# Kernel tuning notes

Measured on AMD Instinct MI355X. Metric: run time of the kernel, lower is better.

Reference implementation:

```python
import jax, jax.numpy as jnp
import numpy as np

J = 15       # joints
D = 128      # per-joint feature dim
ANG = 3      # per-joint angle dim
EPS = 1e-12  # F.normalize eps
TEMP = 200.0
SCALE = 16.0


def setup_inputs() -> dict:
    key = jax.random.key(0)
    k1, k2 = jax.random.split(key)
    B, N, E = 16384, 68, J * D + J * ANG  # E = 1965
    emb = jax.random.normal(k1, (B, E), dtype=jnp.float32)
    W = jax.random.normal(k2, (N, E), dtype=jnp.float32)
    return {"emb": emb, "W": W}


def reference(emb, W):
    B = emb.shape[0]
    N = W.shape[0]
    # split feature / angle blocks
    x_feat = emb[:, : J * D].reshape(B, J, D)        # (B, 15, 128)
    x_ang = emb[:, J * D :].reshape(B, 1, J, ANG)    # (B, 1, 15, 3)
    p_feat = W[:, : J * D].reshape(N, J, D)          # (N, 15, 128)
    p_ang = W[:, J * D :].reshape(1, N, J, ANG)      # (1, N, 15, 3)

    # per-joint angle distance and (detached in torch) softmax weighting
    ang_w = jnp.linalg.norm(x_ang - p_ang, axis=-1)            # (B, N, 15)
    w2 = jax.nn.softmax(ang_w / TEMP, axis=-1) * J             # (B, N, 15)

    # NOTE: the torch code computes argsort(ang_w) but immediately overwrites the
    # index with an identity permutation (ind = [0..14]), so the gather is a no-op.
    # Hence normalization is over the flat 15*128 block per batch / per class.
    xn = x_feat / jnp.maximum(
        jnp.linalg.norm(x_feat.reshape(B, -1), axis=-1), EPS
    )[:, None, None]
    pn = p_feat / jnp.maximum(
        jnp.linalg.norm(p_feat.reshape(N, -1), axis=-1), EPS
    )[:, None, None]

    # per-joint cosine contributions, weighted and summed
    s = jnp.einsum("bjd,njd->bnj", xn, pn)                     # (B, N, 15)
    logit = (s * w2).sum(-1) * SCALE                           # (B, N)
    return logit
```

## Files before the change

### kernel.cpp

```cpp
#include <hip/hip_runtime.h>
#include <hip/hip_bf16.h>

typedef __bf16 bf16x8 __attribute__((ext_vector_type(8)));
typedef float  f32x4  __attribute__((ext_vector_type(4)));

static constexpr int E    = 1965;
static constexpr int KF   = 1920;
static constexpr int NJ   = 15;
static constexpr int NCLS = 68;
static constexpr int NPAD = 80;
static constexpr int NT   = 5;
static constexpr int NS   = 60;
static constexpr int CH   = 12;

static constexpr size_t PNF_BYTES = (size_t)NT * NS * 64 * 8 * 2;

__global__ __launch_bounds__(256) void prep_kernel(const float* __restrict__ W,
                                                   __bf16* __restrict__ pnf,
                                                   float* __restrict__ pa) {
    const int n = blockIdx.x;
    const int t = threadIdx.x;
    float v[8];
    float ss = 0.f;
    if (n < NCLS && t < 240) {
        const float* src = W + (size_t)n * E + 8 * t;
        #pragma unroll
        for (int i = 0; i < 8; ++i) { v[i] = src[i]; ss += v[i] * v[i]; }
    } else {
        #pragma unroll
        for (int i = 0; i < 8; ++i) v[i] = 0.f;
    }
    #pragma unroll
    for (int off = 32; off >= 1; off >>= 1) ss += __shfl_xor(ss, off);
    __shared__ float rbuf[4];
    if ((t & 63) == 0) rbuf[t >> 6] = ss;
    __syncthreads();
    const float total = rbuf[0] + rbuf[1] + rbuf[2] + rbuf[3];
    const float rnorm = 1.f / fmaxf(sqrtf(total), 1e-12f);

    if (t < 240) {
        bf16x8 o;
        #pragma unroll
        for (int i = 0; i < 8; ++i) o[i] = (__bf16)(v[i] * rnorm);
        const int s = t >> 2, g = t & 3;
        const int lane = (n & 15) + 16 * g;
        const size_t off = (((size_t)(n >> 4) * NS + s) * 64 + lane) * 8;
        *(bf16x8*)(pnf + off) = o;
    }
    if (t < 45) {
        pa[n * 45 + t] = (n < NCLS) ? W[(size_t)n * E + KF + t] : 0.f;
    }
}

__global__ __launch_bounds__(320) void cos_kernel(const float* __restrict__ emb,
                                                  const __bf16* __restrict__ pnf,
                                                  const float* __restrict__ pa,
                                                  float* __restrict__ out) {
    __shared__ float  Abuf[2][2560];
    __shared__ __bf16 Bbuf[2][25][512];
    __shared__ float  xa[16][48];

    const int tid = threadIdx.x;
    const int m0  = blockIdx.x * 16;
    const int w   = tid >> 6;
    const int l   = tid & 63;
    const int lr  = l & 15;
    const int lg  = l >> 4;

    for (int idx = tid; idx < 16 * 45; idx += 320) {
        const int r = idx / 45, c = idx - r * 45;
        xa[r][c] = emb[(size_t)(m0 + r) * E + KF + c];
    }

    const int gA   = l ^ ((l >> 3) & 7);
    const int arow = (gA >> 1) & 15;
    const float* srcA = emb + (size_t)(m0 + arow) * E + 8 * (gA >> 5) + 4 * (gA & 1)
                        + 32 * w;
    const __bf16* srcB = pnf + ((size_t)w * NS * 64 + l) * 8;

    #define ISSUE(c, buf)                                                               \
        {                                                                               \
            _Pragma("unroll")                                                           \
            for (int b_ = 0; b_ < 2; ++b_)                                              \
                __builtin_amdgcn_global_load_lds(                                       \
                    (const __attribute__((address_space(1))) void*)(srcA + 160 * (c) + 16 * b_), \
                    (__attribute__((address_space(3))) void*)&Abuf[buf][(2 * w + b_) * 256],     \
                    16, 0, 0);                                                          \
            _Pragma("unroll")                                                           \
            for (int s_ = 0; s_ < 5; ++s_)                                              \
                __builtin_amdgcn_global_load_lds(                                       \
                    (const __attribute__((address_space(1))) void*)(srcB + (5 * (c) + s_) * 512),\
                    (__attribute__((address_space(3))) void*)&Bbuf[buf][w * 5 + s_][0],          \
                    16, 0, 0);                                                          \
        }

    const int g0    = 32 * (lg & 1) + 2 * lr;
    const int p_lo  = g0 ^ ((g0 >> 3) & 7);
    const int p_hi  = p_lo ^ 1;
    const int aoff_lo = (lg >> 1) * 256 + 4 * p_lo;
    const int aoff_hi = (lg >> 1) * 256 + 4 * p_hi;

    f32x4 acc[NJ];
    #pragma unroll
    for (int j = 0; j < NJ; ++j) acc[j] = f32x4{0.f, 0.f, 0.f, 0.f};
    float ssq = 0.f;

    ISSUE(0, 0);

    #pragma unroll
    for (int c = 0; c < CH; ++c) {
        __syncthreads();
        if (c + 1 < CH) ISSUE(c + 1, (c + 1) & 1);

        #pragma unroll
        for (int s = 0; s < 5; ++s) {
            const f32x4 alo = *(const f32x4*)&Abuf[c & 1][s * 512 + aoff_lo];
            const f32x4 ahi = *(const f32x4*)&Abuf[c & 1][s * 512 + aoff_hi];
            const bf16x8 b  = *(const bf16x8*)&Bbuf[c & 1][w * 5 + s][l * 8];
            bf16x8 af;
            #pragma unroll
            for (int q = 0; q < 4; ++q) {
                ssq += alo[q] * alo[q] + ahi[q] * ahi[q];
                af[q]     = (__bf16)alo[q];
                af[4 + q] = (__bf16)ahi[q];
            }
            const int gk = 5 * c + s;
            acc[gk >> 2] = __builtin_amdgcn_mfma_f32_16x16x32_bf16(af, b, acc[gk >> 2], 0, 0, 0);
        }
    }
    #undef ISSUE

    ssq += __shfl_xor(ssq, 16);
    ssq += __shfl_xor(ssq, 32);

    const int r0  = lg * 4;
    const int col = w * 16 + lr;

    float rn[4];
    #pragma unroll
    for (int r = 0; r < 4; ++r)
        rn[r] = 240.f / fmaxf(sqrtf(__shfl(ssq, r0 + r)), 1e-12f);

    const float* pav = pa + col * 45;
    float num[4] = {0.f, 0.f, 0.f, 0.f};
    float den[4] = {0.f, 0.f, 0.f, 0.f};
    #pragma unroll
    for (int j = 0; j < NJ; ++j) {
        const float p0a = pav[3 * j + 0];
        const float p1a = pav[3 * j + 1];
        const float p2a = pav[3 * j + 2];
        #pragma unroll
        for (int r = 0; r < 4; ++r) {
            const float d0 = xa[r0 + r][3 * j + 0] - p0a;
            const float d1 = xa[r0 + r][3 * j + 1] - p1a;
            const float d2 = xa[r0 + r][3 * j + 2] - p2a;
            const float dist = sqrtf(d0 * d0 + d1 * d1 + d2 * d2);
            const float e = __expf(dist * 0.005f);
            den[r] += e;
            num[r] += e * acc[j][r];
        }
    }

    if (col < NCLS) {
        #pragma unroll
        for (int r = 0; r < 4; ++r)
            out[(size_t)(m0 + r0 + r) * NCLS + col] = rn[r] * num[r] / den[r];
    }
}

extern "C" void kernel_launch(void* const* d_in, const int* in_sizes, int n_in,
                              void* d_out, int out_size, void* d_ws, size_t ws_size,
                              hipStream_t stream) {
    const float* emb = (const float*)d_in[0];
    const float* W   = (const float*)d_in[1];
    float* out = (float*)d_out;
    __bf16* pnf = (__bf16*)d_ws;
    float*  pa  = (float*)((char*)d_ws + PNF_BYTES);
    const int B = in_sizes[0] / E;

    prep_kernel<<<NPAD, 256, 0, stream>>>(W, pnf, pa);
    cos_kernel<<<B / 16, 320, 0, stream>>>(emb, pnf, pa, out);
}
```

Baseline: 88.65 us.

## Use triple-buffered smaller K chunks with explicit vmcnt waits and raw barriers

Replaces the double-buffered 12-chunk loop (5 K-steps per chunk) with a triple-buffered 30-chunk loop (2 K-steps per chunk) that prefetches two chunks ahead. It uses s_waitcnt vmcnt counts and s_barrier with sched_barriers instead of __syncthreads, and simplifies the A layout so only 4 of the 5 waves load A. The aim is to keep more loads in flight and shrink per-block LDS so more blocks fit per CU. The cost is more barriers per block and manually counted waits that must stay in step with how many loads each wave issues.

```diff
diff --git a/kernel.cpp b/kernel.cpp
--- a/kernel.cpp
+++ b/kernel.cpp
@@ -11,7 +11,8 @@
 static constexpr int NPAD = 80;
 static constexpr int NT   = 5;
 static constexpr int NS   = 60;
-static constexpr int CH   = 12;
+static constexpr int CH   = 30;
+static constexpr int NBUF = 3;
 
 static constexpr size_t PNF_BYTES = (size_t)NT * NS * 64 * 8 * 2;
 
@@ -56,8 +57,8 @@
                                                   const __bf16* __restrict__ pnf,
                                                   const float* __restrict__ pa,
                                                   float* __restrict__ out) {
-    __shared__ float  Abuf[2][2560];
-    __shared__ __bf16 Bbuf[2][25][512];
+    __shared__ f32x4  Abuf[NBUF][2][2][64];
+    __shared__ __bf16 Bbuf[NBUF][NT][2][512];
     __shared__ float  xa[16][48];
 
     const int tid = threadIdx.x;
@@ -71,52 +72,50 @@
         const int r = idx / 45, c = idx - r * 45;
         xa[r][c] = emb[(size_t)(m0 + r) * E + KF + c];
     }
+    asm volatile("s_waitcnt lgkmcnt(0)" ::: "memory");
 
-    const int gA   = l ^ ((l >> 3) & 7);
-    const int arow = (gA >> 1) & 15;
-    const float* srcA = emb + (size_t)(m0 + arow) * E + 8 * (gA >> 5) + 4 * (gA & 1)
-                        + 32 * w;
+    const float* srcA = emb + (size_t)(m0 + lr) * E + 8 * lg + 32 * (w >> 1) + 4 * (w & 1);
     const __bf16* srcB = pnf + ((size_t)w * NS * 64 + l) * 8;
 
-    #define ISSUE(c, buf)                                                               \
-        {                                                                               \
-            _Pragma("unroll")                                                           \
-            for (int b_ = 0; b_ < 2; ++b_)                                              \
-                __builtin_amdgcn_global_load_lds(                                       \
-                    (const __attribute__((address_space(1))) void*)(srcA + 160 * (c) + 16 * b_), \
-                    (__attribute__((address_space(3))) void*)&Abuf[buf][(2 * w + b_) * 256],     \
-                    16, 0, 0);                                                          \
-            _Pragma("unroll")                                                           \
-            for (int s_ = 0; s_ < 5; ++s_)                                              \
-                __builtin_amdgcn_global_load_lds(                                       \
-                    (const __attribute__((address_space(1))) void*)(srcB + (5 * (c) + s_) * 512),\
-                    (__attribute__((address_space(3))) void*)&Bbuf[buf][w * 5 + s_][0],          \
-                    16, 0, 0);                                                          \
+    #define ISSUE(c)                                                                     \
+        {                                                                                \
+            if (w < 4)                                                                   \
+                __builtin_amdgcn_global_load_lds(                                        \
+                    (const __attribute__((address_space(1))) void*)(srcA + 64 * (c)),    \
+                    (__attribute__((address_space(3))) void*)&Abuf[(c) % NBUF][w >> 1][w & 1][0], \
+                    16, 0, 0);                                                           \
+            _Pragma("unroll")                                                            \
+            for (int s_ = 0; s_ < 2; ++s_)                                               \
+                __builtin_amdgcn_global_load_lds(                                        \
+                    (const __attribute__((address_space(1))) void*)(srcB + (2 * (c) + s_) * 512), \
+                    (__attribute__((address_space(3))) void*)&Bbuf[(c) % NBUF][w][s_][0],         \
+                    16, 0, 0);                                                           \
         }
-
-    const int g0    = 32 * (lg & 1) + 2 * lr;
-    const int p_lo  = g0 ^ ((g0 >> 3) & 7);
-    const int p_hi  = p_lo ^ 1;
-    const int aoff_lo = (lg >> 1) * 256 + 4 * p_lo;
-    const int aoff_hi = (lg >> 1) * 256 + 4 * p_hi;
 
     f32x4 acc[NJ];
     #pragma unroll
     for (int j = 0; j < NJ; ++j) acc[j] = f32x4{0.f, 0.f, 0.f, 0.f};
     float ssq = 0.f;
 
-    ISSUE(0, 0);
+    ISSUE(0);
+    ISSUE(1);
 
     #pragma unroll
     for (int c = 0; c < CH; ++c) {
-        __syncthreads();
-        if (c + 1 < CH) ISSUE(c + 1, (c + 1) & 1);
+        if (c == CH - 1)  { asm volatile("s_waitcnt vmcnt(0)" ::: "memory"); }
+        else if (w < 4)   { asm volatile("s_waitcnt vmcnt(3)" ::: "memory"); }
+        else              { asm volatile("s_waitcnt vmcnt(2)" ::: "memory"); }
+        __builtin_amdgcn_sched_barrier(0);
+        __builtin_amdgcn_s_barrier();
+        __builtin_amdgcn_sched_barrier(0);
+        if (c + 2 < CH) ISSUE(c + 2);
+        __builtin_amdgcn_sched_barrier(0);
 
         #pragma unroll
-        for (int s = 0; s < 5; ++s) {
-            const f32x4 alo = *(const f32x4*)&Abuf[c & 1][s * 512 + aoff_lo];
-            const f32x4 ahi = *(const f32x4*)&Abuf[c & 1][s * 512 + aoff_hi];
-            const bf16x8 b  = *(const bf16x8*)&Bbuf[c & 1][w * 5 + s][l * 8];
+        for (int s = 0; s < 2; ++s) {
+            const f32x4 alo = Abuf[c % NBUF][s][0][l];
+            const f32x4 ahi = Abuf[c % NBUF][s][1][l];
+            const bf16x8 b  = *(const bf16x8*)&Bbuf[c % NBUF][w][s][l * 8];
             bf16x8 af;
             #pragma unroll
             for (int q = 0; q < 4; ++q) {
@@ -124,7 +123,7 @@
                 af[q]     = (__bf16)alo[q];
                 af[4 + q] = (__bf16)ahi[q];
             }
-            const int gk = 5 * c + s;
+            const int gk = 2 * c + s;
             acc[gk >> 2] = __builtin_amdgcn_mfma_f32_16x16x32_bf16(af, b, acc[gk >> 2], 0, 0, 0);
         }
     }
```

Measured after the change: 255.6 us. 188% more time.
